# Kernel tuning notes

Hardware: AMD Instinct MI355X
Metric: run time of the kernel (lower is better)

The kernel has to match this reference:

```python
import jax, jax.numpy as jnp
import numpy as np

N_NODES = 50000
N_EDGES = 400000
CH = 256
NNZ_ADJ = 800000
NNZ_INC = 800000

def _spmm(rows, cols, vals, xw, num_segments):
    # y = S @ xw where S is COO-sparse [num_segments, xw.shape[0]]
    return jax.ops.segment_sum(vals[:, None] * xw[cols], rows, num_segments=num_segments)

def setup_inputs() -> dict:
    key = jax.random.key(0)
    ks = jax.random.split(key, 10)
    scale = 1.0 / np.sqrt(CH)
    return {
        "x": jax.random.normal(ks[0], (N_NODES, CH), dtype=jnp.float32),
        "adj_rows": jax.random.randint(ks[1], (NNZ_ADJ,), 0, N_NODES, dtype=jnp.int32),
        "adj_cols": jax.random.randint(ks[2], (NNZ_ADJ,), 0, N_NODES, dtype=jnp.int32),
        "adj_vals": jnp.ones((NNZ_ADJ,), dtype=jnp.float32),
        "inc_rows": jax.random.randint(ks[3], (NNZ_INC,), 0, N_NODES, dtype=jnp.int32),
        "inc_cols": jax.random.randint(ks[4], (NNZ_INC,), 0, N_EDGES, dtype=jnp.int32),
        "inc_vals": jnp.ones((NNZ_INC,), dtype=jnp.float32),
        "W00": jax.random.normal(ks[5], (CH, CH), dtype=jnp.float32) * scale,
        "W01": jax.random.normal(ks[6], (CH, CH), dtype=jnp.float32) * scale,
        "W10": jax.random.normal(ks[7], (CH, CH), dtype=jnp.float32) * scale,
        "W11": jax.random.normal(ks[8], (CH, CH), dtype=jnp.float32) * scale,
    }

def reference(x, adj_rows, adj_cols, adj_vals, inc_rows, inc_cols, inc_vals, W00, W01, W10, W11):
    # Level 1: nodes->nodes via A0 (sigmoid), nodes->edges via B1^T (sigmoid)
    x_nodes_l1 = jax.nn.sigmoid(_spmm(adj_rows, adj_cols, adj_vals, x @ W00, N_NODES))
    # B1^T: rows are edge indices (inc_cols), cols are node indices (inc_rows)
    x_edges_l1 = jax.nn.sigmoid(_spmm(inc_cols, inc_rows, inc_vals, x @ W01, N_EDGES))
    # Level 2: no update activation
    x_nodes_l2 = _spmm(adj_rows, adj_cols, adj_vals, x_nodes_l1 @ W10, N_NODES)
    x_edges_l2 = _spmm(inc_rows, inc_cols, inc_vals, x_edges_l1 @ W11, N_NODES)
    # Merge on nodes: sum + sigmoid
    return jax.nn.sigmoid(x_nodes_l2 + x_edges_l2)
```

## Files before the change

kernel.cpp:

```cpp
#include <hip/hip_runtime.h>
#include <math.h>

#define N_NODES 50000
#define N_EDGES 400000
#define CH      256
#define NNZ     800000

typedef short s16x8 __attribute__((ext_vector_type(8)));
typedef float f32x4 __attribute__((ext_vector_type(4)));

__device__ __forceinline__ float sigmoidf_(float x) {
    return 1.0f / (1.0f + __expf(-x));
}
__device__ __forceinline__ unsigned short f2bf(float f) {
    unsigned u = __float_as_uint(f);
    u = (u + 0x7FFFu + ((u >> 16) & 1u)) >> 16;
    return (unsigned short)u;
}
__device__ __forceinline__ float bf2f(unsigned short h) {
    return __uint_as_float((unsigned)h << 16);
}
__device__ __forceinline__ f32x4 bfrow(ushort4 s) {
    f32x4 r;
    r.x = bf2f(s.x); r.y = bf2f(s.y); r.z = bf2f(s.z); r.w = bf2f(s.w);
    return r;
}

__global__ __launch_bounds__(256) void fill_i32(int* __restrict__ p, int val, int n)
{
    int stride = gridDim.x * 256;
    for (int i = blockIdx.x * 256 + threadIdx.x; i < n; i += stride) p[i] = val;
}

__global__ __launch_bounds__(256) void hist_cvt(
    const int* __restrict__ k0, int* __restrict__ c0, int* __restrict__ r0,
    const int* __restrict__ k1, int* __restrict__ c1, int* __restrict__ r1,
    const int* __restrict__ k2, int* __restrict__ c2, int* __restrict__ r2, int n,
    const float* __restrict__ W00, const float* __restrict__ W01,
    const float* __restrict__ W10, const float* __restrict__ W11,
    unsigned short* __restrict__ T0, unsigned short* __restrict__ T1,
    unsigned short* __restrict__ Wh10, unsigned short* __restrict__ Wl10,
    unsigned short* __restrict__ Wh11, unsigned short* __restrict__ Wl11)
{
    int y = blockIdx.y;
    if (y < 3) {
        int i = blockIdx.x * 256 + threadIdx.x;
        if (i >= n) return;
        if      (y == 0) r0[i] = atomicAdd(&c0[k0[i]], 1);
        else if (y == 1) r1[i] = atomicAdd(&c1[k1[i]], 1);
        else             r2[i] = atomicAdd(&c2[k2[i]], 1);
        return;
    }
    int x = blockIdx.x;
    if (x >= 1024) return;
    int variant = x >> 8, nn = x & 255, k = threadIdx.x;
    if (variant == 0) { T0[nn * 256 + k] = f2bf(W00[k * 256 + nn]); return; }
    if (variant == 1) { T1[nn * 256 + k] = f2bf(W01[k * 256 + nn]); return; }
    const float* W = (variant == 2) ? W10 : W11;
    unsigned short* Th = (variant == 2) ? Wh10 : Wh11;
    unsigned short* Tl = (variant == 2) ? Wl10 : Wl11;
    float w = W[k * 256 + nn];
    unsigned short h = f2bf(w);
    int k0i = k >> 5, g = (k >> 3) & 3, j = k & 7;
    size_t o = (((size_t)(k0i * 4 + g)) * 256 + nn) * 8 + j;
    Th[o] = h;
    Tl[o] = f2bf(w - bf2f(h));
}

__global__ __launch_bounds__(256) void reserve3(
    int* __restrict__ c0, int* __restrict__ sd0, int n0,
    int* __restrict__ c1, int* __restrict__ sd1, int n1,
    int* __restrict__ c2, int* __restrict__ sd2, int n2,
    int* __restrict__ cursors)
{
    int y = blockIdx.y;
    int* cnt = (y == 0) ? c0 : (y == 1) ? c1 : c2;
    int* sd  = (y == 0) ? sd0 : (y == 1) ? sd1 : sd2;
    int  nk  = (y == 0) ? n0 : (y == 1) ? n1 : n2;
    int k = blockIdx.x * 256 + threadIdx.x;
    if (k >= nk) return;
    int deg  = cnt[k];
    int base = deg ? atomicAdd(&cursors[y], deg) : 0;
    sd[k]  = base | (deg << 20);
    cnt[k] = base;
}

__global__ __launch_bounds__(256) void scatter3(
    const int* __restrict__ k0, const int* __restrict__ o0, const float* __restrict__ v0,
    const int* __restrict__ c0, const int* __restrict__ r0, int2* __restrict__ cv0,
    const int* __restrict__ k1, const int* __restrict__ o1, const float* __restrict__ v1,
    const int* __restrict__ c1, const int* __restrict__ r1, int2* __restrict__ cv1,
    const int* __restrict__ k2, const int* __restrict__ o2, const float* __restrict__ v2,
    const int* __restrict__ c2, const int* __restrict__ r2, int2* __restrict__ cv2,
    const int* __restrict__ sd_e, int n)
{
    int i = blockIdx.x * 256 + threadIdx.x;
    if (i >= n) return;
    if (blockIdx.y == 0) {
        int pos = c0[k0[i]] + r0[i];
        cv0[pos] = make_int2(o0[i], __float_as_int(v0[i]));
    } else if (blockIdx.y == 1) {
        int pos = c1[k1[i]] + r1[i];
        cv1[pos] = make_int2(o1[i], __float_as_int(v1[i]));
    } else {
        int pos = c2[k2[i]] + r2[i];
        cv2[pos] = make_int2(sd_e[o2[i]], __float_as_int(v2[i]));
    }
}

__global__ __launch_bounds__(256, 2) void mfma_gemm2(
    const float* __restrict__ X,
    const unsigned short* __restrict__ Wt0, const unsigned short* __restrict__ Wt1,
    unsigned short* __restrict__ Y0, unsigned short* __restrict__ Y1, int M)
{
    const int wv = threadIdx.x >> 6, lane = threadIdx.x & 63;
    const int row0 = blockIdx.x * 64 + wv * 16;
    const int r = lane & 15, g = lane >> 4;

    f32x4 acc0[16], acc1[16];
#pragma unroll
    for (int t = 0; t < 16; t++) {
        acc0[t] = (f32x4){0.f, 0.f, 0.f, 0.f};
        acc1[t] = (f32x4){0.f, 0.f, 0.f, 0.f};
    }

    int arow = row0 + r; if (arow >= M) arow = M - 1;

#pragma unroll
    for (int k0 = 0; k0 < 256; k0 += 32) {
        const float* xp = X + (size_t)arow * CH + k0 + g * 8;
        float4 f0 = *(const float4*)(xp);
        float4 f1 = *(const float4*)(xp + 4);
        s16x8 a;
        a[0] = f2bf(f0.x); a[1] = f2bf(f0.y); a[2] = f2bf(f0.z); a[3] = f2bf(f0.w);
        a[4] = f2bf(f1.x); a[5] = f2bf(f1.y); a[6] = f2bf(f1.z); a[7] = f2bf(f1.w);
#pragma unroll
        for (int t = 0; t < 16; t++) {
            size_t wo = (size_t)(t * 16 + r) * CH + k0 + g * 8;
            s16x8 b0 = *(const s16x8*)(Wt0 + wo);
            acc0[t] = __builtin_amdgcn_mfma_f32_16x16x32_bf16(a, b0, acc0[t], 0, 0, 0);
            s16x8 b1 = *(const s16x8*)(Wt1 + wo);
            acc1[t] = __builtin_amdgcn_mfma_f32_16x16x32_bf16(a, b1, acc1[t], 0, 0, 0);
        }
    }

    const int drow0 = row0 + g * 4;
#pragma unroll
    for (int t = 0; t < 16; t++) {
        int col = t * 16 + r;
#pragma unroll
        for (int j = 0; j < 4; j++) {
            int dr = drow0 + j;
            if (dr < M) {
                Y0[(size_t)dr * CH + col] = f2bf(acc0[t][j]);
                Y1[(size_t)dr * CH + col] = f2bf(acc1[t][j]);
            }
        }
    }
}

__global__ __launch_bounds__(256) void gather_csr(
    const int* __restrict__ sd, const int2* __restrict__ cv,
    const unsigned short* __restrict__ S,
    void* __restrict__ O, int n_rows, int sig, int out_bf)
{
    int r    = (int)((blockIdx.x * 256u + threadIdx.x) >> 6);
    int lane = threadIdx.x & 63;
    if (r >= n_rows) return;
    r = __builtin_amdgcn_readfirstlane(r);

    unsigned sdv = (unsigned)sd[r];
    int base = (int)(sdv & 0xFFFFFu), deg = (int)(sdv >> 20);
    const unsigned lb = (unsigned)lane << 3;
    const char* Sb = (const char*)S;

    f32x4 acc = (f32x4){0.f, 0.f, 0.f, 0.f};
    int i = 0;
    for (; i + 8 <= deg; i += 8) {
        int2 e[8]; ushort4 s[8];
#pragma unroll
        for (int q = 0; q < 8; q++) e[q] = cv[base + i + q];
#pragma unroll
        for (int q = 0; q < 8; q++)
            s[q] = *(const ushort4*)(Sb + (((unsigned)e[q].x << 9) + lb));
#pragma unroll
        for (int q = 0; q < 8; q++) {
            float v = __int_as_float(e[q].y);
            f32x4 vv = {v, v, v, v};
            acc = __builtin_elementwise_fma(vv, bfrow(s[q]), acc);
        }
    }
    for (; i + 4 <= deg; i += 4) {
        int2 e[4]; ushort4 s[4];
#pragma unroll
        for (int q = 0; q < 4; q++) e[q] = cv[base + i + q];
#pragma unroll
        for (int q = 0; q < 4; q++)
            s[q] = *(const ushort4*)(Sb + (((unsigned)e[q].x << 9) + lb));
#pragma unroll
        for (int q = 0; q < 4; q++) {
            float v = __int_as_float(e[q].y);
            f32x4 vv = {v, v, v, v};
            acc = __builtin_elementwise_fma(vv, bfrow(s[q]), acc);
        }
    }
    for (; i < deg; i++) {
        int2 e = cv[base + i];
        float v = __int_as_float(e.y);
        ushort4 s = *(const ushort4*)(Sb + (((unsigned)e.x << 9) + lb));
        f32x4 vv = {v, v, v, v};
        acc = __builtin_elementwise_fma(vv, bfrow(s), acc);
    }
    if (sig) {
        acc.x = sigmoidf_(acc.x); acc.y = sigmoidf_(acc.y);
        acc.z = sigmoidf_(acc.z); acc.w = sigmoidf_(acc.w);
    }
    if (out_bf) {
        ushort4 o; o.x = f2bf(acc.x); o.y = f2bf(acc.y); o.z = f2bf(acc.z); o.w = f2bf(acc.w);
        *(ushort4*)((char*)O + (((unsigned)r << 9) + lb)) = o;
    } else {
        *(f32x4*)((char*)O + (((unsigned)r << 10) + (lb << 1))) = acc;
    }
}

__global__ __launch_bounds__(256) void edge_gather_csr(
    const int* __restrict__ sd_n, const int2* __restrict__ cv_n,
    const int2* __restrict__ cv_e,
    const unsigned short* __restrict__ B, float* __restrict__ F, int n_nodes)
{
    int n    = (int)((blockIdx.x * 256u + threadIdx.x) >> 6);
    int lane = threadIdx.x & 63;
    if (n >= n_nodes) return;
    n = __builtin_amdgcn_readfirstlane(n);

    unsigned sdn = (unsigned)sd_n[n];
    int baseN = (int)(sdn & 0xFFFFFu), degN = (int)(sdn >> 20);
    const unsigned lb = (unsigned)lane << 3;
    const char* Bb = (const char*)B;

    f32x4 acc = (f32x4){0.f, 0.f, 0.f, 0.f};
    for (int i = 0; i < degN; i++) {
        int2 en = cv_n[baseN + i];
        unsigned sde = (unsigned)en.x;
        float v = __int_as_float(en.y);
        int baseE = (int)(sde & 0xFFFFFu), degE = (int)(sde >> 20);

        f32x4 d = (f32x4){0.f, 0.f, 0.f, 0.f};
        int j = 0;
        for (; j + 2 <= degE; j += 2) {
            int2 e0 = cv_e[baseE + j], e1 = cv_e[baseE + j + 1];
            ushort4 b0 = *(const ushort4*)(Bb + (((unsigned)e0.x << 9) + lb));
            ushort4 b1 = *(const ushort4*)(Bb + (((unsigned)e1.x << 9) + lb));
            float u0 = __int_as_float(e0.y), u1 = __int_as_float(e1.y);
            f32x4 uv0 = {u0, u0, u0, u0};
            f32x4 uv1 = {u1, u1, u1, u1};
            d = __builtin_elementwise_fma(uv0, bfrow(b0), d);
            d = __builtin_elementwise_fma(uv1, bfrow(b1), d);
        }
        for (; j < degE; j++) {
            int2 e0 = cv_e[baseE + j];
            float u = __int_as_float(e0.y);
            ushort4 b = *(const ushort4*)(Bb + (((unsigned)e0.x << 9) + lb));
            f32x4 uv = {u, u, u, u};
            d = __builtin_elementwise_fma(uv, bfrow(b), d);
        }
        f32x4 sd4;
        sd4.x = sigmoidf_(d.x); sd4.y = sigmoidf_(d.y);
        sd4.z = sigmoidf_(d.z); sd4.w = sigmoidf_(d.w);
        f32x4 vv = {v, v, v, v};
        acc = __builtin_elementwise_fma(vv, sd4, acc);
    }
    *(f32x4*)((char*)F + (((unsigned)n << 10) + (lb << 1))) = acc;
}

__device__ __forceinline__ void split8(float4 a, float4 b, s16x8& hi, s16x8& lo)
{
    float v[8] = {a.x, a.y, a.z, a.w, b.x, b.y, b.z, b.w};
#pragma unroll
    for (int i = 0; i < 8; i++) {
        unsigned short h = f2bf(v[i]);
        hi[i] = (short)h;
        lo[i] = (short)f2bf(v[i] - bf2f(h));
    }
}

__global__ __launch_bounds__(256, 2) void final_mfma(
    const float* __restrict__ E, const float* __restrict__ F,
    const unsigned short* __restrict__ Wh10, const unsigned short* __restrict__ Wl10,
    const unsigned short* __restrict__ Wh11, const unsigned short* __restrict__ Wl11,
    float* __restrict__ Y, int M)
{
    __shared__ unsigned short lds[4 * 4 * 257 * 8];
    const int tid = threadIdx.x;
    const int wv = tid >> 6, lane = tid & 63;
    const int row0 = blockIdx.x * 128 + wv * 32;
    const int r = lane & 15, g = lane >> 4;

    f32x4 acc[2][16];
#pragma unroll
    for (int gr = 0; gr < 2; gr++)
#pragma unroll
        for (int t = 0; t < 16; t++) acc[gr][t] = (f32x4){0.f, 0.f, 0.f, 0.f};

    int ar0 = row0 + r;      if (ar0 >= M) ar0 = M - 1;
    int ar1 = row0 + 16 + r; if (ar1 >= M) ar1 = M - 1;

    for (int k0i = 0; k0i < 8; ++k0i) {
        const int kbase = k0i * 32 + g * 8;
        const float* p = E + (size_t)ar0 * CH + kbase;
        float4 e0a = *(const float4*)p, e0b = *(const float4*)(p + 4);
        p = E + (size_t)ar1 * CH + kbase;
        float4 e1a = *(const float4*)p, e1b = *(const float4*)(p + 4);
        p = F + (size_t)ar0 * CH + kbase;
        float4 f0a = *(const float4*)p, f0b = *(const float4*)(p + 4);
        p = F + (size_t)ar1 * CH + kbase;
        float4 f1a = *(const float4*)p, f1b = *(const float4*)(p + 4);

        if (k0i) __syncthreads();
#pragma unroll
        for (int m = 0; m < 4; m++) {
            const unsigned short* src =
                (m == 0) ? Wh10 : (m == 1) ? Wl10 : (m == 2) ? Wh11 : Wl11;
            src += (size_t)k0i * 1024 * 8;
#pragma unroll
            for (int g2 = 0; g2 < 4; g2++) {
                int frag = (m * 4 + g2) * 257 + tid;
                *(s16x8*)&lds[frag * 8] = *(const s16x8*)(src + (size_t)(g2 * 256 + tid) * 8);
            }
        }
        __syncthreads();

        s16x8 eh0, el0, eh1, el1, fh0, fl0, fh1, fl1;
        split8(e0a, e0b, eh0, el0);
        split8(e1a, e1b, eh1, el1);
        split8(f0a, f0b, fh0, fl0);
        split8(f1a, f1b, fh1, fl1);

#pragma unroll
        for (int t = 0; t < 16; t++) {
            int rr = t * 16 + r;
            s16x8 bh0 = *(const s16x8*)&lds[((0 + g) * 257 + rr) * 8];
            s16x8 bl0 = *(const s16x8*)&lds[((4 + g) * 257 + rr) * 8];
            s16x8 bh1 = *(const s16x8*)&lds[((8 + g) * 257 + rr) * 8];
            s16x8 bl1 = *(const s16x8*)&lds[((12 + g) * 257 + rr) * 8];

            acc[0][t] = __builtin_amdgcn_mfma_f32_16x16x32_bf16(eh0, bh0, acc[0][t], 0, 0, 0);
            acc[0][t] = __builtin_amdgcn_mfma_f32_16x16x32_bf16(el0, bh0, acc[0][t], 0, 0, 0);
            acc[0][t] = __builtin_amdgcn_mfma_f32_16x16x32_bf16(eh0, bl0, acc[0][t], 0, 0, 0);
            acc[0][t] = __builtin_amdgcn_mfma_f32_16x16x32_bf16(fh0, bh1, acc[0][t], 0, 0, 0);
            acc[0][t] = __builtin_amdgcn_mfma_f32_16x16x32_bf16(fl0, bh1, acc[0][t], 0, 0, 0);
            acc[0][t] = __builtin_amdgcn_mfma_f32_16x16x32_bf16(fh0, bl1, acc[0][t], 0, 0, 0);

            acc[1][t] = __builtin_amdgcn_mfma_f32_16x16x32_bf16(eh1, bh0, acc[1][t], 0, 0, 0);
            acc[1][t] = __builtin_amdgcn_mfma_f32_16x16x32_bf16(el1, bh0, acc[1][t], 0, 0, 0);
            acc[1][t] = __builtin_amdgcn_mfma_f32_16x16x32_bf16(eh1, bl0, acc[1][t], 0, 0, 0);
            acc[1][t] = __builtin_amdgcn_mfma_f32_16x16x32_bf16(fh1, bh1, acc[1][t], 0, 0, 0);
            acc[1][t] = __builtin_amdgcn_mfma_f32_16x16x32_bf16(fl1, bh1, acc[1][t], 0, 0, 0);
            acc[1][t] = __builtin_amdgcn_mfma_f32_16x16x32_bf16(fh1, bl1, acc[1][t], 0, 0, 0);
        }
    }

#pragma unroll
    for (int gr = 0; gr < 2; gr++) {
        const int drow0 = row0 + gr * 16 + g * 4;
#pragma unroll
        for (int t = 0; t < 16; t++) {
            int col = t * 16 + r;
#pragma unroll
            for (int j = 0; j < 4; j++) {
                int dr = drow0 + j;
                if (dr < M) Y[(size_t)dr * CH + col] = sigmoidf_(acc[gr][t][j]);
            }
        }
    }
}

extern "C" void kernel_launch(void* const* d_in, const int* in_sizes, int n_in,
                              void* d_out, int out_size, void* d_ws, size_t ws_size,
                              hipStream_t stream)
{
    const float* x        = (const float*)d_in[0];
    const int*   adj_rows = (const int*)  d_in[1];
    const int*   adj_cols = (const int*)  d_in[2];
    const float* adj_vals = (const float*)d_in[3];
    const int*   inc_rows = (const int*)  d_in[4];
    const int*   inc_cols = (const int*)  d_in[5];
    const float* inc_vals = (const float*)d_in[6];
    const float* W00      = (const float*)d_in[7];
    const float* W01      = (const float*)d_in[8];
    const float* W10      = (const float*)d_in[9];
    const float* W11      = (const float*)d_in[10];

    const size_t SZ_AB = (size_t)N_NODES * CH * 2;
    const size_t SZ_F  = (size_t)N_NODES * CH * 4;
    char* ws = (char*)d_ws;
    size_t off = 0;
    unsigned short* A_bf = (unsigned short*)(ws + off); off += SZ_AB;
    float*          F    = (float*)(ws + off);          off += SZ_F;
    int*   sd_a  = (int*)(ws + off);  off += (size_t)N_NODES * 4;
    int2*  cv_a  = (int2*)(ws + off); off += (size_t)NNZ * 8;
    int*   cursors = (int*)(ws + off); off += 256;
    unsigned short* Wt00  = (unsigned short*)(ws + off); off += (size_t)CH * CH * 2;
    unsigned short* Wt01  = (unsigned short*)(ws + off); off += (size_t)CH * CH * 2;
    unsigned short* Wh10  = (unsigned short*)(ws + off); off += (size_t)CH * CH * 2;
    unsigned short* Wl10  = (unsigned short*)(ws + off); off += (size_t)CH * CH * 2;
    unsigned short* Wh11  = (unsigned short*)(ws + off); off += (size_t)CH * CH * 2;
    unsigned short* Wl11  = (unsigned short*)(ws + off); off += (size_t)CH * CH * 2;
    char* scratch = ws + off;
    int*   cnt_a  = (int*)(scratch);
    int*   cnt_e  = cnt_a + N_NODES;
    int*   cnt_n  = cnt_e + N_EDGES;
    int*   sd_n   = cnt_n + N_NODES;
    int*   sd_e   = sd_n + N_NODES;
    int2*  cv_n   = (int2*)(sd_e + N_EDGES);
    int2*  cv_e   = cv_n + NNZ;
    int*   rank_a = (int*)(cv_e + NNZ);
    int*   rank_e = rank_a + NNZ;
    int*   rank_n = rank_e + NNZ;
    unsigned short* C_bf = (unsigned short*)scratch;
    unsigned short* B_bf = (unsigned short*)d_out;
    float* E = (float*)d_out;

    const int gemm_blocks  = (N_NODES + 63) / 64;
    const int final_blocks = (N_NODES + 127) / 128;
    const int row_blocks   = (N_NODES * 64 + 255) / 256;
    const int ent_blocks   = (NNZ + 255) / 256;
    const int key_blocks   = (N_EDGES + 255) / 256;

    fill_i32<<<1024, 256, 0, stream>>>(cnt_a, 0, N_NODES + N_EDGES + N_NODES);
    fill_i32<<<1, 64, 0, stream>>>(cursors, 0, 3);
    hist_cvt<<<dim3(ent_blocks, 4), 256, 0, stream>>>(
        adj_rows, cnt_a, rank_a, inc_cols, cnt_e, rank_e, inc_rows, cnt_n, rank_n, NNZ,
        W00, W01, W10, W11, Wt00, Wt01, Wh10, Wl10, Wh11, Wl11);
    reserve3<<<dim3(key_blocks, 3), 256, 0, stream>>>(
        cnt_a, sd_a, N_NODES, cnt_e, sd_e, N_EDGES, cnt_n, sd_n, N_NODES, cursors);
    scatter3<<<dim3(ent_blocks, 3), 256, 0, stream>>>(
        adj_rows, adj_cols, adj_vals, cnt_a, rank_a, cv_a,
        inc_cols, inc_rows, inc_vals, cnt_e, rank_e, cv_e,
        inc_rows, inc_cols, inc_vals, cnt_n, rank_n, cv_n, sd_e, NNZ);

    mfma_gemm2<<<gemm_blocks, 256, 0, stream>>>(x, Wt00, Wt01, A_bf, B_bf, N_NODES);

    edge_gather_csr<<<row_blocks, 256, 0, stream>>>(sd_n, cv_n, cv_e,
                                                    B_bf, F, N_NODES);

    gather_csr<<<row_blocks, 256, 0, stream>>>(sd_a, cv_a,
                                               A_bf, C_bf, N_NODES, 1, 1);

    gather_csr<<<row_blocks, 256, 0, stream>>>(sd_a, cv_a,
                                               C_bf, E, N_NODES, 0, 0);

    final_mfma<<<final_blocks, 256, 0, stream>>>(E, F, Wh10, Wl10, Wh11, Wl11,
                                                 (float*)d_out, N_NODES);
}
```

Baseline: 751.8 us.

## Stage packed GEMM weights in LDS and merge cursor zeroing into one fill

The first GEMM now stores W00/W01 in a fragment-packed bf16 layout and copies each 32-wide K slice of both weight matrices into padded shared memory once per block. The MFMA B operands are then read from LDS instead of every wave loading them separately from global memory. The cursors array moves into the zeroed scratch region so a single fill launch clears it, dropping one tiny kernel launch. In exchange, each K step adds two block barriers and the LDS copy is not overlapped with compute.

```diff
diff --git a/kernel.cpp b/kernel.cpp
--- a/kernel.cpp
+++ b/kernel.cpp
@@ -38,7 +38,7 @@
     const int* __restrict__ k2, int* __restrict__ c2, int* __restrict__ r2, int n,
     const float* __restrict__ W00, const float* __restrict__ W01,
     const float* __restrict__ W10, const float* __restrict__ W11,
-    unsigned short* __restrict__ T0, unsigned short* __restrict__ T1,
+    unsigned short* __restrict__ Wp00, unsigned short* __restrict__ Wp01,
     unsigned short* __restrict__ Wh10, unsigned short* __restrict__ Wl10,
     unsigned short* __restrict__ Wh11, unsigned short* __restrict__ Wl11)
 {
@@ -54,15 +54,15 @@
     int x = blockIdx.x;
     if (x >= 1024) return;
     int variant = x >> 8, nn = x & 255, k = threadIdx.x;
-    if (variant == 0) { T0[nn * 256 + k] = f2bf(W00[k * 256 + nn]); return; }
-    if (variant == 1) { T1[nn * 256 + k] = f2bf(W01[k * 256 + nn]); return; }
+    int k0i = k >> 5, g = (k >> 3) & 3, j = k & 7;
+    size_t o = (((size_t)(k0i * 4 + g)) * 256 + nn) * 8 + j;
+    if (variant == 0) { Wp00[o] = f2bf(W00[k * 256 + nn]); return; }
+    if (variant == 1) { Wp01[o] = f2bf(W01[k * 256 + nn]); return; }
     const float* W = (variant == 2) ? W10 : W11;
     unsigned short* Th = (variant == 2) ? Wh10 : Wh11;
     unsigned short* Tl = (variant == 2) ? Wl10 : Wl11;
     float w = W[k * 256 + nn];
     unsigned short h = f2bf(w);
-    int k0i = k >> 5, g = (k >> 3) & 3, j = k & 7;
-    size_t o = (((size_t)(k0i * 4 + g)) * 256 + nn) * 8 + j;
     Th[o] = h;
     Tl[o] = f2bf(w - bf2f(h));
 }
@@ -110,10 +110,12 @@
 
 __global__ __launch_bounds__(256, 2) void mfma_gemm2(
     const float* __restrict__ X,
-    const unsigned short* __restrict__ Wt0, const unsigned short* __restrict__ Wt1,
+    const unsigned short* __restrict__ Wp0, const unsigned short* __restrict__ Wp1,
     unsigned short* __restrict__ Y0, unsigned short* __restrict__ Y1, int M)
 {
-    const int wv = threadIdx.x >> 6, lane = threadIdx.x & 63;
+    __shared__ unsigned short lds[2 * 4 * 257 * 8];
+    const int tid = threadIdx.x;
+    const int wv = tid >> 6, lane = tid & 63;
     const int row0 = blockIdx.x * 64 + wv * 16;
     const int r = lane & 15, g = lane >> 4;
 
@@ -126,20 +128,34 @@
 
     int arow = row0 + r; if (arow >= M) arow = M - 1;
 
-#pragma unroll
-    for (int k0 = 0; k0 < 256; k0 += 32) {
-        const float* xp = X + (size_t)arow * CH + k0 + g * 8;
+    for (int k0i = 0; k0i < 8; ++k0i) {
+        const float* xp = X + (size_t)arow * CH + k0i * 32 + g * 8;
         float4 f0 = *(const float4*)(xp);
         float4 f1 = *(const float4*)(xp + 4);
+
+        if (k0i) __syncthreads();
+#pragma unroll
+        for (int m = 0; m < 2; m++) {
+            const unsigned short* src = (m == 0) ? Wp0 : Wp1;
+            src += (size_t)k0i * 1024 * 8;
+#pragma unroll
+            for (int g2 = 0; g2 < 4; g2++) {
+                int frag = (m * 4 + g2) * 257 + tid;
+                *(s16x8*)&lds[frag * 8] = *(const s16x8*)(src + (size_t)(g2 * 256 + tid) * 8);
+            }
+        }
+        __syncthreads();
+
         s16x8 a;
         a[0] = f2bf(f0.x); a[1] = f2bf(f0.y); a[2] = f2bf(f0.z); a[3] = f2bf(f0.w);
         a[4] = f2bf(f1.x); a[5] = f2bf(f1.y); a[6] = f2bf(f1.z); a[7] = f2bf(f1.w);
+
 #pragma unroll
         for (int t = 0; t < 16; t++) {
-            size_t wo = (size_t)(t * 16 + r) * CH + k0 + g * 8;
-            s16x8 b0 = *(const s16x8*)(Wt0 + wo);
+            int rr = t * 16 + r;
+            s16x8 b0 = *(const s16x8*)&lds[((0 + g) * 257 + rr) * 8];
+            s16x8 b1 = *(const s16x8*)&lds[((4 + g) * 257 + rr) * 8];
             acc0[t] = __builtin_amdgcn_mfma_f32_16x16x32_bf16(a, b0, acc0[t], 0, 0, 0);
-            s16x8 b1 = *(const s16x8*)(Wt1 + wo);
             acc1[t] = __builtin_amdgcn_mfma_f32_16x16x32_bf16(a, b1, acc1[t], 0, 0, 0);
         }
     }
@@ -399,24 +415,24 @@
     float*          F    = (float*)(ws + off);          off += SZ_F;
     int*   sd_a  = (int*)(ws + off);  off += (size_t)N_NODES * 4;
     int2*  cv_a  = (int2*)(ws + off); off += (size_t)NNZ * 8;
-    int*   cursors = (int*)(ws + off); off += 256;
-    unsigned short* Wt00  = (unsigned short*)(ws + off); off += (size_t)CH * CH * 2;
-    unsigned short* Wt01  = (unsigned short*)(ws + off); off += (size_t)CH * CH * 2;
+    unsigned short* Wp00  = (unsigned short*)(ws + off); off += (size_t)CH * CH * 2;
+    unsigned short* Wp01  = (unsigned short*)(ws + off); off += (size_t)CH * CH * 2;
     unsigned short* Wh10  = (unsigned short*)(ws + off); off += (size_t)CH * CH * 2;
     unsigned short* Wl10  = (unsigned short*)(ws + off); off += (size_t)CH * CH * 2;
     unsigned short* Wh11  = (unsigned short*)(ws + off); off += (size_t)CH * CH * 2;
     unsigned short* Wl11  = (unsigned short*)(ws + off); off += (size_t)CH * CH * 2;
     char* scratch = ws + off;
-    int*   cnt_a  = (int*)(scratch);
-    int*   cnt_e  = cnt_a + N_NODES;
-    int*   cnt_n  = cnt_e + N_EDGES;
-    int*   sd_n   = cnt_n + N_NODES;
-    int*   sd_e   = sd_n + N_NODES;
-    int2*  cv_n   = (int2*)(sd_e + N_EDGES);
-    int2*  cv_e   = cv_n + NNZ;
-    int*   rank_a = (int*)(cv_e + NNZ);
-    int*   rank_e = rank_a + NNZ;
-    int*   rank_n = rank_e + NNZ;
+    int*   cnt_a   = (int*)(scratch);
+    int*   cnt_e   = cnt_a + N_NODES;
+    int*   cnt_n   = cnt_e + N_EDGES;
+    int*   cursors = cnt_n + N_NODES;
+    int*   sd_n    = cursors + 64;
+    int*   sd_e    = sd_n + N_NODES;
+    int2*  cv_n    = (int2*)(sd_e + N_EDGES);
+    int2*  cv_e    = cv_n + NNZ;
+    int*   rank_a  = (int*)(cv_e + NNZ);
+    int*   rank_e  = rank_a + NNZ;
+    int*   rank_n  = rank_e + NNZ;
     unsigned short* C_bf = (unsigned short*)scratch;
     unsigned short* B_bf = (unsigned short*)d_out;
     float* E = (float*)d_out;
@@ -427,11 +443,10 @@
     const int ent_blocks   = (NNZ + 255) / 256;
     const int key_blocks   = (N_EDGES + 255) / 256;
 
-    fill_i32<<<1024, 256, 0, stream>>>(cnt_a, 0, N_NODES + N_EDGES + N_NODES);
-    fill_i32<<<1, 64, 0, stream>>>(cursors, 0, 3);
+    fill_i32<<<1024, 256, 0, stream>>>(cnt_a, 0, N_NODES + N_EDGES + N_NODES + 64);
     hist_cvt<<<dim3(ent_blocks, 4), 256, 0, stream>>>(
         adj_rows, cnt_a, rank_a, inc_cols, cnt_e, rank_e, inc_rows, cnt_n, rank_n, NNZ,
-        W00, W01, W10, W11, Wt00, Wt01, Wh10, Wl10, Wh11, Wl11);
+        W00, W01, W10, W11, Wp00, Wp01, Wh10, Wl10, Wh11, Wl11);
     reserve3<<<dim3(key_blocks, 3), 256, 0, stream>>>(
         cnt_a, sd_a, N_NODES, cnt_e, sd_e, N_EDGES, cnt_n, sd_n, N_NODES, cursors);
     scatter3<<<dim3(ent_blocks, 3), 256, 0, stream>>>(
@@ -439,7 +454,7 @@
         inc_cols, inc_rows, inc_vals, cnt_e, rank_e, cv_e,
         inc_rows, inc_cols, inc_vals, cnt_n, rank_n, cv_n, sd_e, NNZ);
 
-    mfma_gemm2<<<gemm_blocks, 256, 0, stream>>>(x, Wt00, Wt01, A_bf, B_bf, N_NODES);
+    mfma_gemm2<<<gemm_blocks, 256, 0, stream>>>(x, Wp00, Wp01, A_bf, B_bf, N_NODES);
 
     edge_gather_csr<<<row_blocks, 256, 0, stream>>>(sd_n, cv_n, cv_e,
                                                     B_bf, F, N_NODES);
```

Result: faster. 658.7 us (-12.4%).
